# Optimization experiments

Hardware: AMD Instinct MI355X
Metric: run time of the kernel (lower is better)

The kernel has to match this reference:

```python
import jax, jax.numpy as jnp
import numpy as np

N = 10000
DIM = 64
F_CONST = 1.0
B_CONST = 0.1
R_CONST = 0.01


def setup_inputs() -> dict:
    key = jax.random.key(0)
    k1, k2 = jax.random.split(key)
    t = jnp.zeros((1,), dtype=jnp.float32)  # autonomous system; t unused
    x = jax.random.uniform(k1, (N, DIM), dtype=jnp.float32)
    A = jax.random.uniform(k2, (N, N), dtype=jnp.float32)
    return {"t": t, "x": x, "A": A}


def reference(t, x, A):
    # dx/dt = f - b*x - diag(A @ (r * x x^T)).reshape(-1, 1)
    # diag(A @ x x^T)_i = sum_j A_ij <x_j, x_i> = <x_i, (A @ x)_i>
    # so the interaction term is r * rowsum(x * (A @ x)) -- same math, no NxN intermediate.
    Ax = A @ x                                        # [N, DIM]
    outer = R_CONST * jnp.sum(x * Ax, axis=1, keepdims=True)  # [N, 1]
    return F_CONST - B_CONST * x - outer              # [N, DIM] via broadcast
```

## Files before the change

### kernel.cpp

```cpp
#include <hip/hip_runtime.h>
#include <stdint.h>


#define N_ROWS 10000
#define DIM 64
#define KTILE 32
#define NKT 320
#define KSPLIT 2
#define TPW 40
#define PF 4
#define F_CONST 1.0f
#define B_CONST 0.1f
#define R_CONST 0.01f

#define SACC_OFF_BYTES 1310720

typedef __attribute__((ext_vector_type(8))) short s16x8;
typedef __attribute__((ext_vector_type(4))) float f32x4;
typedef __attribute__((ext_vector_type(4))) uint32_t u32x4;

__device__ __forceinline__ uint32_t pack_bf16(float a, float b) {
    uint32_t ua = __builtin_bit_cast(uint32_t, a);
    uint32_t ub = __builtin_bit_cast(uint32_t, b);
    ua += 0x7FFFu + ((ua >> 16) & 1u);
    ub += 0x7FFFu + ((ub >> 16) & 1u);
    return (ua >> 16) | (ub & 0xFFFF0000u);
}

__device__ __forceinline__ s16x8 pack_frag(f32x4 lo, f32x4 hi) {
    u32x4 p;
    p.x = pack_bf16(lo.x, lo.y);
    p.y = pack_bf16(lo.z, lo.w);
    p.z = pack_bf16(hi.x, hi.y);
    p.w = pack_bf16(hi.z, hi.w);
    return __builtin_bit_cast(s16x8, p);
}

__global__ __launch_bounds__(256) void pack_x_kernel(const float* __restrict__ x,
                                                     uint32_t* __restrict__ ws,
                                                     float* __restrict__ sacc) {
    int id = blockIdx.x * 256 + threadIdx.x;
    if (id < N_ROWS) sacc[id] = 0.0f;
    int frag = id >> 6;
    int L = id & 63;
    int t = frag >> 2;
    int c = frag & 3;
    int k0 = t * KTILE + (L >> 4) * 8;
    int col = c * 16 + (L & 15);
    float v[8];
#pragma unroll
    for (int j = 0; j < 8; ++j) {
        int k = k0 + j;
        v[j] = (k < N_ROWS) ? x[k * DIM + col] : 0.0f;
    }
    u32x4 p;
    p.x = pack_bf16(v[0], v[1]);
    p.y = pack_bf16(v[2], v[3]);
    p.z = pack_bf16(v[4], v[5]);
    p.w = pack_bf16(v[6], v[7]);
    ((u32x4*)ws)[id] = p;
}

__global__ __launch_bounds__(256, 4) void gemm_dot_kernel(
    const float* __restrict__ A, const float* __restrict__ x,
    const uint32_t* __restrict__ ws, float* __restrict__ sacc) {
    int tid = threadIdx.x;
    int w = tid >> 6;
    int L = tid & 63;
    int quad = L >> 4;
    int m = L & 15;
    int rbase = blockIdx.x * 16;
    int t0 = (blockIdx.y * 4 + w) * TPW;

    const float* Ar = A + (size_t)(rbase + m) * N_ROWS;
    const u32x4* pb = (const u32x4*)ws;

    auto aload = [&](int t, f32x4& lo, f32x4& hi) {
        int k = t * KTILE + quad * 8;
        if (k > N_ROWS - 8) k = N_ROWS - 8;
        lo = __builtin_nontemporal_load((const f32x4*)(Ar + k));
        hi = __builtin_nontemporal_load((const f32x4*)(Ar + k + 4));
    };
    auto bload = [&](int t, int cc) -> u32x4 {
        return pb[(size_t)t * 256 + cc * 64 + L];
    };

    f32x4 acc[4] = {{0.f, 0.f, 0.f, 0.f},
                    {0.f, 0.f, 0.f, 0.f},
                    {0.f, 0.f, 0.f, 0.f},
                    {0.f, 0.f, 0.f, 0.f}};

    f32x4 alo[PF], ahi[PF];
    u32x4 bb[2][4];

#pragma unroll
    for (int u = 0; u < PF; ++u) aload(t0 + u, alo[u], ahi[u]);
#pragma unroll
    for (int cc = 0; cc < 4; ++cc) bb[0][cc] = bload(t0, cc);
#pragma unroll
    for (int cc = 0; cc < 4; ++cc) bb[1][cc] = bload(t0 + 1, cc);

    for (int tb = 0; tb < TPW; tb += PF) {
#pragma unroll
        for (int u = 0; u < PF; ++u) {
            int i = tb + u;
            int t = t0 + i;
            s16x8 af = pack_frag(alo[u], ahi[u]);
#pragma unroll
            for (int cc = 0; cc < 4; ++cc)
                acc[cc] = __builtin_amdgcn_mfma_f32_16x16x32_bf16(
                    af, __builtin_bit_cast(s16x8, bb[u & 1][cc]), acc[cc], 0, 0, 0);
            if (i + 2 < TPW) {
#pragma unroll
                for (int cc = 0; cc < 4; ++cc) bb[u & 1][cc] = bload(t + 2, cc);
            }
            if (i + PF < TPW)
                aload(t + PF, alo[u], ahi[u]);
        }
    }

    float pr[4];
#pragma unroll
    for (int r = 0; r < 4; ++r) {
        int grow = rbase + quad * 4 + r;
        const float* xr = x + (size_t)grow * DIM + m;
        pr[r] = acc[0][r] * xr[0] + acc[1][r] * xr[16] +
                acc[2][r] * xr[32] + acc[3][r] * xr[48];
        pr[r] += __shfl_xor(pr[r], 1);
        pr[r] += __shfl_xor(pr[r], 2);
        pr[r] += __shfl_xor(pr[r], 4);
        pr[r] += __shfl_xor(pr[r], 8);
    }
    if (m == 0) {
#pragma unroll
        for (int r = 0; r < 4; ++r)
            atomicAdd(&sacc[rbase + quad * 4 + r], pr[r]);
    }
}

__global__ __launch_bounds__(256) void finalize_kernel(const float* __restrict__ x,
                                                       const float* __restrict__ sacc,
                                                       float* __restrict__ out) {
    int id = blockIdx.x * 256 + threadIdx.x;
    f32x4 xv = ((const f32x4*)x)[id];
    float s = R_CONST * sacc[id >> 4];
    f32x4 o;
    o.x = F_CONST - B_CONST * xv.x - s;
    o.y = F_CONST - B_CONST * xv.y - s;
    o.z = F_CONST - B_CONST * xv.z - s;
    o.w = F_CONST - B_CONST * xv.w - s;
    ((f32x4*)out)[id] = o;
}

extern "C" void kernel_launch(void* const* d_in, const int* in_sizes, int n_in,
                              void* d_out, int out_size, void* d_ws, size_t ws_size,
                              hipStream_t stream) {
    const float* x = (const float*)d_in[1];
    const float* A = (const float*)d_in[2];
    float* out = (float*)d_out;
    uint32_t* ws = (uint32_t*)d_ws;
    float* sacc = (float*)((char*)d_ws + SACC_OFF_BYTES);

    pack_x_kernel<<<320, 256, 0, stream>>>(x, ws, sacc);
    gemm_dot_kernel<<<dim3(625, KSPLIT), 256, 0, stream>>>(A, x, ws, sacc);
    finalize_kernel<<<625, 256, 0, stream>>>(x, sacc, out);
}
```

Before: 587.3 us.

## Stage A tiles into LDS via direct global-to-LDS loads with double buffering

Replaces per-lane register loads of A, which touched 32-byte pieces across 16 strided rows, with wave-wide global_load_lds copies. Each copy brings a contiguous 1 KB slice of a row into XOR-swizzled, double-buffered shared memory. Each block now walks half of K in chunks of 256 columns, and the four waves split the 8 k-tiles of each chunk instead of each wave owning its own K range. The aim is better coalescing and deeper memory-level parallelism on the bandwidth-bound A stream. The cost is two block barriers per chunk and more LDS use, which may limit occupancy.

```diff
diff --git a/kernel.cpp b/kernel.cpp
--- a/kernel.cpp
+++ b/kernel.cpp
@@ -6,9 +6,9 @@
 #define DIM 64
 #define KTILE 32
 #define NKT 320
-#define KSPLIT 2
-#define TPW 40
-#define PF 4
+#define CHUNK_K 256
+#define NCHUNK 20
+#define KHALF 5120
 #define F_CONST 1.0f
 #define B_CONST 0.1f
 #define R_CONST 0.01f
@@ -64,59 +64,65 @@
 __global__ __launch_bounds__(256, 4) void gemm_dot_kernel(
     const float* __restrict__ A, const float* __restrict__ x,
     const uint32_t* __restrict__ ws, float* __restrict__ sacc) {
+    __shared__ __align__(16) float lds[2][16 * CHUNK_K];
+
     int tid = threadIdx.x;
     int w = tid >> 6;
     int L = tid & 63;
     int quad = L >> 4;
     int m = L & 15;
     int rbase = blockIdx.x * 16;
-    int t0 = (blockIdx.y * 4 + w) * TPW;
-
-    const float* Ar = A + (size_t)(rbase + m) * N_ROWS;
+    int half = blockIdx.y;
+    const float* Ab = A + (size_t)rbase * N_ROWS;
     const u32x4* pb = (const u32x4*)ws;
 
-    auto aload = [&](int t, f32x4& lo, f32x4& hi) {
-        int k = t * KTILE + quad * 8;
-        if (k > N_ROWS - 8) k = N_ROWS - 8;
-        lo = __builtin_nontemporal_load((const f32x4*)(Ar + k));
-        hi = __builtin_nontemporal_load((const f32x4*)(Ar + k + 4));
-    };
-    auto bload = [&](int t, int cc) -> u32x4 {
-        return pb[(size_t)t * 256 + cc * 64 + L];
+    auto stage = [&](int c, int b) {
+#pragma unroll
+        for (int i = 0; i < 4; ++i) {
+            int row = w * 4 + i;
+            int col = half * KHALF + c * CHUNK_K + ((L ^ (row & 7)) << 2);
+            if (col > N_ROWS - 4) col = N_ROWS - 4;
+            __builtin_amdgcn_global_load_lds(
+                (const __attribute__((address_space(1))) uint32_t*)(Ab + (size_t)row * N_ROWS + col),
+                (__attribute__((address_space(3))) uint32_t*)(&lds[b][row * CHUNK_K]),
+                16, 0, 0);
+        }
     };
 
     f32x4 acc[4] = {{0.f, 0.f, 0.f, 0.f},
                     {0.f, 0.f, 0.f, 0.f},
                     {0.f, 0.f, 0.f, 0.f},
                     {0.f, 0.f, 0.f, 0.f}};
+    u32x4 bb[8];
 
-    f32x4 alo[PF], ahi[PF];
-    u32x4 bb[2][4];
+    stage(0, 0);
+    int b = 0;
+    for (int c = 0; c < NCHUNK; ++c) {
+        int T0 = half * (NKT / 2) + c * 8;
+#pragma unroll
+        for (int cc = 0; cc < 4; ++cc) bb[cc] = pb[(size_t)(T0 + w) * 256 + cc * 64 + L];
+#pragma unroll
+        for (int cc = 0; cc < 4; ++cc) bb[4 + cc] = pb[(size_t)(T0 + w + 4) * 256 + cc * 64 + L];
+        __builtin_amdgcn_sched_barrier(0);
+        if (c + 1 < NCHUNK) stage(c + 1, b ^ 1);
+        asm volatile("s_waitcnt vmcnt(4)" ::: "memory");
+        __builtin_amdgcn_s_barrier();
 
 #pragma unroll
-    for (int u = 0; u < PF; ++u) aload(t0 + u, alo[u], ahi[u]);
-#pragma unroll
-    for (int cc = 0; cc < 4; ++cc) bb[0][cc] = bload(t0, cc);
-#pragma unroll
-    for (int cc = 0; cc < 4; ++cc) bb[1][cc] = bload(t0 + 1, cc);
-
-    for (int tb = 0; tb < TPW; tb += PF) {
-#pragma unroll
-        for (int u = 0; u < PF; ++u) {
-            int i = tb + u;
-            int t = t0 + i;
-            s16x8 af = pack_frag(alo[u], ahi[u]);
+        for (int u = 0; u < 2; ++u) {
+            int tt = w + 4 * u;
+            int u0 = tt * 8 + quad * 2;
+            const char* base = (const char*)&lds[b][0] + m * (CHUNK_K * 4);
+            f32x4 lo = *(const f32x4*)(base + (((u0) ^ (m & 7)) << 4));
+            f32x4 hi = *(const f32x4*)(base + (((u0 + 1) ^ (m & 7)) << 4));
+            s16x8 af = pack_frag(lo, hi);
 #pragma unroll
             for (int cc = 0; cc < 4; ++cc)
                 acc[cc] = __builtin_amdgcn_mfma_f32_16x16x32_bf16(
-                    af, __builtin_bit_cast(s16x8, bb[u & 1][cc]), acc[cc], 0, 0, 0);
-            if (i + 2 < TPW) {
-#pragma unroll
-                for (int cc = 0; cc < 4; ++cc) bb[u & 1][cc] = bload(t + 2, cc);
-            }
-            if (i + PF < TPW)
-                aload(t + PF, alo[u], ahi[u]);
+                    af, __builtin_bit_cast(s16x8, bb[u * 4 + cc]), acc[cc], 0, 0, 0);
         }
+        __builtin_amdgcn_s_barrier();
+        b ^= 1;
     }
 
     float pr[4];
@@ -162,6 +168,6 @@
     float* sacc = (float*)((char*)d_ws + SACC_OFF_BYTES);
 
     pack_x_kernel<<<320, 256, 0, stream>>>(x, ws, sacc);
-    gemm_dot_kernel<<<dim3(625, KSPLIT), 256, 0, stream>>>(A, x, ws, sacc);
+    gemm_dot_kernel<<<dim3(625, 2), 256, 0, stream>>>(A, x, ws, sacc);
     finalize_kernel<<<625, 256, 0, stream>>>(x, sacc, out);
 }
```

Result: faster. 541.3 us (-7.8%).
